# Optimization experiments

Hardware: AMD Instinct MI355X
Metric: run time of the kernel (lower is better)

## Reference

```python
import jax, jax.numpy as jnp
import numpy as np

N_NODES = 50000
N_EDGES = 800000


def setup_inputs() -> dict:
    key = jax.random.key(0)
    k1, k2, k3, k4 = jax.random.split(key, 4)
    x = jax.random.normal(k1, (N_NODES, 128), dtype=jnp.float32)
    edge_index = jax.random.randint(k2, (2, N_EDGES), 0, N_NODES, dtype=jnp.int64)
    W1 = jax.random.normal(k3, (128, 64), dtype=jnp.float32) / np.sqrt(128.0)
    b1 = jnp.zeros((64,), dtype=jnp.float32)
    W2 = jax.random.normal(k4, (64, 40), dtype=jnp.float32) / np.sqrt(64.0)
    b2 = jnp.zeros((40,), dtype=jnp.float32)
    return {"x": x, "edge_index": edge_index, "W1": W1, "b1": b1, "W2": W2, "b2": b2}


def _gcn_norm(edge_index, n_nodes):
    # Add self-loops, then compute symmetric normalization D^{-1/2} A D^{-1/2}
    loop = jnp.arange(n_nodes, dtype=edge_index.dtype)
    row = jnp.concatenate([edge_index[0], loop])  # source
    col = jnp.concatenate([edge_index[1], loop])  # target
    ones = jnp.ones(row.shape[0], dtype=jnp.float32)
    deg = jax.ops.segment_sum(ones, col, num_segments=n_nodes)
    dinv = jnp.where(deg > 0, jax.lax.rsqrt(deg), 0.0)
    norm = dinv[row] * dinv[col]  # [E + N]
    return row, col, norm


def _gcn_conv(h, W, b, row, col, norm, n_nodes):
    hw = h @ W                         # transform first (smaller messages)
    msg = hw[row] * norm[:, None]      # gather + scale per edge
    agg = jax.ops.segment_sum(msg, col, num_segments=n_nodes)
    return agg + b


def reference(x, edge_index, W1, b1, W2, b2):
    n = x.shape[0]
    row, col, norm = _gcn_norm(edge_index, n)
    h = _gcn_conv(x, W1, b1, row, col, norm, n)
    h = jax.nn.relu(h)
    h = _gcn_conv(h, W2, b2, row, col, norm, n)
    return jax.nn.softmax(h, axis=-1)
```

## Files before the change

kernel.cpp:

```cpp
#include <hip/hip_runtime.h>
#include <hip/hip_fp16.h>

#define N_NODES 50000
#define N_EDGES 800000
#define F_IN   128
#define F_MID  64
#define F_OUT  40

#define SLICE_SHIFT 8
#define SLICE_SZ    256
#define NSLICE      196
#define PCHUNKS     256
#define PCHUNK_E    ((N_EDGES + PCHUNKS - 1) / PCHUNKS)
#define NCOUNT      (NSLICE * PCHUNKS)


__global__ __launch_bounds__(256) void bucket_count(const int* __restrict__ ei,
                                                    int* __restrict__ counts) {
    __shared__ int cnt[NSLICE];
    if (threadIdx.x < NSLICE) cnt[threadIdx.x] = 0;
    __syncthreads();
    int e0 = blockIdx.x * PCHUNK_E;
    int e1 = e0 + PCHUNK_E; if (e1 > N_EDGES) e1 = N_EDGES;
    for (int e = e0 + threadIdx.x; e < e1; e += 256) {
        int c = ei[N_EDGES + e];
        atomicAdd(&cnt[c >> SLICE_SHIFT], 1);
    }
    __syncthreads();
    if (threadIdx.x < NSLICE) counts[threadIdx.x * PCHUNKS + blockIdx.x] = cnt[threadIdx.x];
}


__global__ __launch_bounds__(256) void sc_scan(const int* __restrict__ counts,
                                               int* __restrict__ choff) {
    __shared__ int T[256];
    __shared__ int P[256];
    __shared__ int ws[4];
    int tid = threadIdx.x, b = blockIdx.x;
    int lane = tid & 63, wv = tid >> 6;

    for (int r = wv; r < NSLICE; r += 4) {
        const int* row = counts + r * PCHUNKS;
        int ssum = row[lane] + row[lane + 64] + row[lane + 128] + row[lane + 192];
#pragma unroll
        for (int off = 32; off > 0; off >>= 1) ssum += __shfl_xor(ssum, off, 64);
        if (lane == 0) T[r] = ssum;
    }
    if (tid >= NSLICE && tid < 256) T[tid] = 0;
    __syncthreads();

    int v = T[tid];
    int inc = v;
#pragma unroll
    for (int st = 1; st < 64; st <<= 1) {
        int t = __shfl_up(inc, st, 64);
        if (lane >= st) inc += t;
    }
    if (lane == 63) ws[wv] = inc;
    __syncthreads();
    int woff = 0;
    for (int w = 0; w < wv; ++w) woff += ws[w];
    P[tid] = woff + inc - v;
    __syncthreads();
    int base_b = P[b];

    __syncthreads();
    int c = counts[b * PCHUNKS + tid];
    inc = c;
#pragma unroll
    for (int st = 1; st < 64; st <<= 1) {
        int t = __shfl_up(inc, st, 64);
        if (lane >= st) inc += t;
    }
    if (lane == 63) ws[wv] = inc;
    __syncthreads();
    woff = 0;
    for (int w = 0; w < wv; ++w) woff += ws[w];
    choff[b * PCHUNKS + tid] = base_b + woff + inc - c;
}


__global__ __launch_bounds__(256) void bucket_scatter(const int* __restrict__ ei,
                                                      const int* __restrict__ choff,
                                                      int* __restrict__ pairs) {
    __shared__ int cur[NSLICE];
    if (threadIdx.x < NSLICE) cur[threadIdx.x] = choff[threadIdx.x * PCHUNKS + blockIdx.x];
    __syncthreads();
    int e0 = blockIdx.x * PCHUNK_E;
    int e1 = e0 + PCHUNK_E; if (e1 > N_EDGES) e1 = N_EDGES;
    for (int e = e0 + threadIdx.x; e < e1; e += 256) {
        int r = ei[e];
        int c = ei[N_EDGES + e];
        int pos = atomicAdd(&cur[c >> SLICE_SHIFT], 1);
        pairs[pos] = r | ((c & (SLICE_SZ - 1)) << 16);
    }
}


__global__ __launch_bounds__(256) void slice_csr_gemm1(const int* __restrict__ pairs,
                                                       const int* __restrict__ choff,
                                                       const float* __restrict__ x,
                                                       const float* __restrict__ W1,
                                                       int* __restrict__ rowptr,
                                                       float* __restrict__ dinv,
                                                       int* __restrict__ srcs,
                                                       __half* __restrict__ hw1h) {
    __shared__ int hist[SLICE_SZ];
    __shared__ int wpart[4];
    __shared__ float sdinv[SLICE_SZ];
    __shared__ float sW[F_IN * F_MID];
    __shared__ float sX[64][68];
    int s = blockIdx.x;
    int base = choff[s * PCHUNKS];
    int end  = (s == NSLICE - 1) ? N_EDGES : choff[(s + 1) * PCHUNKS];
    int tid = threadIdx.x;
    hist[tid] = 0;
    __syncthreads();
    for (int i = base + tid; i < end; i += 256)
        atomicAdd(&hist[pairs[i] >> 16], 1);
    __syncthreads();
    int v = hist[tid];
    int lane = tid & 63, wv = tid >> 6;
    int inc = v;
#pragma unroll
    for (int st = 1; st < 64; st <<= 1) {
        int t = __shfl_up(inc, st, 64);
        if (lane >= st) inc += t;
    }
    if (lane == 63) wpart[wv] = inc;
    __syncthreads();
    int woff = 0;
    for (int w = 0; w < wv; ++w) woff += wpart[w];
    int ex = woff + inc - v;
    __syncthreads();
    hist[tid] = ex;
    float dv = rsqrtf((float)v + 1.0f);
    sdinv[tid] = dv;
    int node = s * SLICE_SZ + tid;
    if (node < N_NODES) {
        rowptr[node] = base + ex;
        dinv[node]   = dv;
    }
    if (node == N_NODES - 1) rowptr[N_NODES] = N_EDGES;
    __syncthreads();
    for (int i = base + tid; i < end; i += 256) {
        int p = pairs[i];
        int pos = atomicAdd(&hist[p >> 16], 1);
        srcs[base + pos] = p & 0xFFFF;
    }

    const float4* W4 = (const float4*)W1;
    float4* sW4 = (float4*)sW;
    for (int i = tid; i < F_IN * F_MID / 4; i += 256) sW4[i] = W4[i];

    int tx = tid & 15, ty = tid >> 4;
    int c0 = tx * 4, r0 = ty * 4;
    int sBase = s * SLICE_SZ;

    for (int sub = 0; sub < 4; ++sub) {
        int row0 = sBase + sub * 64;
        float acc[4][4] = {};
        for (int p = 0; p < 2; ++p) {
            __syncthreads();
#pragma unroll
            for (int it = 0; it < 4; ++it) {
                int i = (tid + it * 256) * 4;
                int r = i >> 6, k = i & 63;
                float4 vx = make_float4(0.f, 0.f, 0.f, 0.f);
                if (row0 + r < N_NODES)
                    vx = *(const float4*)&x[(size_t)(row0 + r) * F_IN + p * 64 + k];
                *(float4*)&sX[r][k] = vx;
            }
            __syncthreads();
            const float* sWp = sW + p * 64 * F_MID;
#pragma unroll 4
            for (int k = 0; k < 64; ++k) {
                float4 w = *(const float4*)&sWp[k * F_MID + c0];
                float a0 = sX[r0 + 0][k];
                float a1 = sX[r0 + 1][k];
                float a2 = sX[r0 + 2][k];
                float a3 = sX[r0 + 3][k];
                acc[0][0] = fmaf(a0, w.x, acc[0][0]); acc[0][1] = fmaf(a0, w.y, acc[0][1]);
                acc[0][2] = fmaf(a0, w.z, acc[0][2]); acc[0][3] = fmaf(a0, w.w, acc[0][3]);
                acc[1][0] = fmaf(a1, w.x, acc[1][0]); acc[1][1] = fmaf(a1, w.y, acc[1][1]);
                acc[1][2] = fmaf(a1, w.z, acc[1][2]); acc[1][3] = fmaf(a1, w.w, acc[1][3]);
                acc[2][0] = fmaf(a2, w.x, acc[2][0]); acc[2][1] = fmaf(a2, w.y, acc[2][1]);
                acc[2][2] = fmaf(a2, w.z, acc[2][2]); acc[2][3] = fmaf(a2, w.w, acc[2][3]);
                acc[3][0] = fmaf(a3, w.x, acc[3][0]); acc[3][1] = fmaf(a3, w.y, acc[3][1]);
                acc[3][2] = fmaf(a3, w.z, acc[3][2]); acc[3][3] = fmaf(a3, w.w, acc[3][3]);
            }
        }
#pragma unroll
        for (int j = 0; j < 4; ++j) {
            int row = row0 + r0 + j;
            if (row < N_NODES) {
                float d = sdinv[sub * 64 + r0 + j];
                __half2 p0 = __floats2half2_rn(acc[j][0] * d, acc[j][1] * d);
                __half2 p1 = __floats2half2_rn(acc[j][2] * d, acc[j][3] * d);
                uint2 u = make_uint2(*reinterpret_cast<unsigned int*>(&p0),
                                     *reinterpret_cast<unsigned int*>(&p1));
                *reinterpret_cast<uint2*>(&hw1h[(size_t)row * F_MID + c0]) = u;
            }
        }
    }
}


__global__ __launch_bounds__(256) void gather1_kernel(const int* __restrict__ rowptr,
                                                      const int* __restrict__ srcs,
                                                      const __half* __restrict__ hw1h,
                                                      const float* __restrict__ dinv,
                                                      const float* __restrict__ b1,
                                                      float* __restrict__ h) {
    int n = blockIdx.x * 4 + (threadIdx.x >> 6);
    int lane = threadIdx.x & 63;
    if (n >= N_NODES) return;
    int s = __builtin_amdgcn_readfirstlane(rowptr[n]);
    int e = __builtin_amdgcn_readfirstlane(rowptr[n + 1]);
    const __half* hb = hw1h + lane;
    float acc = 0.f;
    int j = s;
    for (; j + 8 <= e; j += 8) {
        int i0 = srcs[j + 0], i1 = srcs[j + 1], i2 = srcs[j + 2], i3 = srcs[j + 3];
        int i4 = srcs[j + 4], i5 = srcs[j + 5], i6 = srcs[j + 6], i7 = srcs[j + 7];
        float v0 = __half2float(hb[(size_t)i0 << 6]);
        float v1 = __half2float(hb[(size_t)i1 << 6]);
        float v2 = __half2float(hb[(size_t)i2 << 6]);
        float v3 = __half2float(hb[(size_t)i3 << 6]);
        float v4 = __half2float(hb[(size_t)i4 << 6]);
        float v5 = __half2float(hb[(size_t)i5 << 6]);
        float v6 = __half2float(hb[(size_t)i6 << 6]);
        float v7 = __half2float(hb[(size_t)i7 << 6]);
        acc += ((v0 + v1) + (v2 + v3)) + ((v4 + v5) + (v6 + v7));
    }
    for (; j + 2 <= e; j += 2) {
        int i0 = srcs[j], i1 = srcs[j + 1];
        acc += __half2float(hb[(size_t)i0 << 6]) + __half2float(hb[(size_t)i1 << 6]);
    }
    if (j < e) acc += __half2float(hb[(size_t)srcs[j] << 6]);
    float d = dinv[n];
    float v = fmaf(d, acc + __half2float(hb[(size_t)n << 6]), b1[lane]);
    h[(size_t)n * F_MID + lane] = fmaxf(v, 0.f);
}


__global__ __launch_bounds__(256) void gemm2_kernel(const float* __restrict__ h,
                                                    const float* __restrict__ W2,
                                                    const float* __restrict__ dinv,
                                                    __half* __restrict__ hw2h) {
    __shared__ float sW[F_MID * F_OUT];
    for (int i = threadIdx.x; i < F_MID * F_OUT; i += 256) sW[i] = W2[i];
    __syncthreads();
    int idx = blockIdx.x * 256 + threadIdx.x;
    int r = idx >> 6;
    int c = idx & 63;
    float acc = 0.f;
    if (c < F_OUT) {
        const float* hr = h + (size_t)r * F_MID;
#pragma unroll
        for (int k = 0; k < F_MID; ++k) acc = fmaf(hr[k], sW[k * F_OUT + c], acc);
        acc *= dinv[r];
    }
    hw2h[idx] = __float2half(acc);
}


__global__ __launch_bounds__(256) void gather2_softmax_kernel(const int* __restrict__ rowptr,
                                                              const int* __restrict__ srcs,
                                                              const __half* __restrict__ hw2h,
                                                              const float* __restrict__ dinv,
                                                              const float* __restrict__ b2,
                                                              float* __restrict__ out) {
    int n = blockIdx.x * 4 + (threadIdx.x >> 6);
    int lane = threadIdx.x & 63;
    if (n >= N_NODES) return;
    int s = __builtin_amdgcn_readfirstlane(rowptr[n]);
    int e = __builtin_amdgcn_readfirstlane(rowptr[n + 1]);
    const __half* gb = hw2h + lane;
    float acc = 0.f;
    int j = s;
    for (; j + 8 <= e; j += 8) {
        int i0 = srcs[j + 0], i1 = srcs[j + 1], i2 = srcs[j + 2], i3 = srcs[j + 3];
        int i4 = srcs[j + 4], i5 = srcs[j + 5], i6 = srcs[j + 6], i7 = srcs[j + 7];
        float v0 = __half2float(gb[(size_t)i0 << 6]);
        float v1 = __half2float(gb[(size_t)i1 << 6]);
        float v2 = __half2float(gb[(size_t)i2 << 6]);
        float v3 = __half2float(gb[(size_t)i3 << 6]);
        float v4 = __half2float(gb[(size_t)i4 << 6]);
        float v5 = __half2float(gb[(size_t)i5 << 6]);
        float v6 = __half2float(gb[(size_t)i6 << 6]);
        float v7 = __half2float(gb[(size_t)i7 << 6]);
        acc += ((v0 + v1) + (v2 + v3)) + ((v4 + v5) + (v6 + v7));
    }
    for (; j + 2 <= e; j += 2) {
        int i0 = srcs[j], i1 = srcs[j + 1];
        acc += __half2float(gb[(size_t)i0 << 6]) + __half2float(gb[(size_t)i1 << 6]);
    }
    if (j < e) acc += __half2float(gb[(size_t)srcs[j] << 6]);
    float d = dinv[n];
    float v = -3.402823466e38f;
    if (lane < F_OUT)
        v = fmaf(d, acc + __half2float(gb[(size_t)n << 6]), b2[lane]);
    float m = v;
#pragma unroll
    for (int off = 32; off > 0; off >>= 1) m = fmaxf(m, __shfl_xor(m, off, 64));
    float p = (lane < F_OUT) ? __expf(v - m) : 0.f;
    float su = p;
#pragma unroll
    for (int off = 32; off > 0; off >>= 1) su += __shfl_xor(su, off, 64);
    if (lane < F_OUT) out[(size_t)n * F_OUT + lane] = p / su;
}


extern "C" void kernel_launch(void* const* d_in, const int* in_sizes, int n_in,
                              void* d_out, int out_size, void* d_ws, size_t ws_size,
                              hipStream_t stream) {
    const float* x  = (const float*)d_in[0];
    const int*   ei = (const int*)d_in[1];
    const float* W1 = (const float*)d_in[2];
    const float* b1 = (const float*)d_in[3];
    const float* W2 = (const float*)d_in[4];
    const float* b2 = (const float*)d_in[5];
    float* out = (float*)d_out;

    char* ws = (char*)d_ws;
    size_t off = 0;
    auto alloc = [&](size_t bytes) -> void* {
        void* p = ws + off;
        off += (bytes + 255) & ~(size_t)255;
        return p;
    };
    int*    counts = (int*)   alloc(NCOUNT * sizeof(int));
    int*    choff  = (int*)   alloc(NCOUNT * sizeof(int));
    int*    pairs  = (int*)   alloc((size_t)N_EDGES * sizeof(int));
    int*    rowptr = (int*)   alloc((N_NODES + 1) * sizeof(int));
    float*  dinv   = (float*) alloc(N_NODES * sizeof(float));
    int*    srcs   = (int*)   alloc((size_t)N_EDGES * sizeof(int));
    __half* hw1h   = (__half*)alloc((size_t)N_NODES * F_MID * sizeof(__half));
    float*  h      = (float*) alloc((size_t)N_NODES * F_MID * sizeof(float));
    __half* hw2h   = (__half*)alloc((size_t)N_NODES * F_MID * sizeof(__half));

    bucket_count   <<<PCHUNKS, 256, 0, stream>>>(ei, counts);
    sc_scan        <<<NSLICE, 256, 0, stream>>>(counts, choff);
    bucket_scatter <<<PCHUNKS, 256, 0, stream>>>(ei, choff, pairs);
    slice_csr_gemm1<<<NSLICE, 256, 0, stream>>>(pairs, choff, x, W1, rowptr, dinv, srcs, hw1h);
    gather1_kernel <<<(N_NODES + 3) / 4, 256, 0, stream>>>(rowptr, srcs, hw1h, dinv, b1, h);
    gemm2_kernel   <<<(N_NODES * F_MID) / 256, 256, 0, stream>>>(h, W2, dinv, hw2h);
    gather2_softmax_kernel<<<(N_NODES + 3) / 4, 256, 0, stream>>>(rowptr, srcs, hw2h, dinv, b2, out);
}
```

Before: 241.6 us.

## Split CSR build from GEMM1 and stage bucket scatter through shared memory

The fused slice_csr_gemm1 kernel ran on only 196 blocks, so the 128x64 GEMM over 50k nodes used few CUs. It is split into a slice_csr kernel and a separate gemm1 kernel with 782 blocks of 64 rows, which reads dinv from global memory. bucket_scatter now does a local prefix sum per chunk, sorts edges by slice in shared memory, and then writes pairs to global in contiguous runs instead of scattering them. The cost is one extra kernel launch and a round trip of dinv through global memory.

```diff
diff --git a/kernel.cpp b/kernel.cpp
--- a/kernel.cpp
+++ b/kernel.cpp
@@ -63,8 +63,8 @@
     P[tid] = woff + inc - v;
     __syncthreads();
     int base_b = P[b];
-
-    __syncthreads();
+    __syncthreads();
+
     int c = counts[b * PCHUNKS + tid];
     inc = c;
 #pragma unroll
@@ -81,35 +81,62 @@
 
 
 __global__ __launch_bounds__(256) void bucket_scatter(const int* __restrict__ ei,
+                                                      const int* __restrict__ counts,
                                                       const int* __restrict__ choff,
                                                       int* __restrict__ pairs) {
+    __shared__ int lofs[NSLICE];
     __shared__ int cur[NSLICE];
-    if (threadIdx.x < NSLICE) cur[threadIdx.x] = choff[threadIdx.x * PCHUNKS + blockIdx.x];
-    __syncthreads();
-    int e0 = blockIdx.x * PCHUNK_E;
+    __shared__ int delta[NSLICE];
+    __shared__ int wsp[4];
+    __shared__ int staged[PCHUNK_E];
+    __shared__ unsigned char sl[PCHUNK_E];
+    int tid = threadIdx.x, b = blockIdx.x;
+    int lane = tid & 63, wv = tid >> 6;
+
+    int c = (tid < NSLICE) ? counts[tid * PCHUNKS + b] : 0;
+    int inc = c;
+#pragma unroll
+    for (int st = 1; st < 64; st <<= 1) {
+        int t = __shfl_up(inc, st, 64);
+        if (lane >= st) inc += t;
+    }
+    if (lane == 63) wsp[wv] = inc;
+    __syncthreads();
+    int woff = 0;
+    for (int w = 0; w < wv; ++w) woff += wsp[w];
+    int ex = woff + inc - c;
+    if (tid < NSLICE) {
+        lofs[tid]  = ex;
+        cur[tid]   = ex;
+        delta[tid] = choff[tid * PCHUNKS + b] - ex;
+    }
+    __syncthreads();
+
+    int e0 = b * PCHUNK_E;
     int e1 = e0 + PCHUNK_E; if (e1 > N_EDGES) e1 = N_EDGES;
-    for (int e = e0 + threadIdx.x; e < e1; e += 256) {
+    int nE = e1 - e0;
+    for (int e = e0 + tid; e < e1; e += 256) {
         int r = ei[e];
-        int c = ei[N_EDGES + e];
-        int pos = atomicAdd(&cur[c >> SLICE_SHIFT], 1);
-        pairs[pos] = r | ((c & (SLICE_SZ - 1)) << 16);
-    }
-}
-
-
-__global__ __launch_bounds__(256) void slice_csr_gemm1(const int* __restrict__ pairs,
-                                                       const int* __restrict__ choff,
-                                                       const float* __restrict__ x,
-                                                       const float* __restrict__ W1,
-                                                       int* __restrict__ rowptr,
-                                                       float* __restrict__ dinv,
-                                                       int* __restrict__ srcs,
-                                                       __half* __restrict__ hw1h) {
+        int cc = ei[N_EDGES + e];
+        int s = cc >> SLICE_SHIFT;
+        int pos = atomicAdd(&cur[s], 1);
+        staged[pos] = r | ((cc & (SLICE_SZ - 1)) << 16);
+        sl[pos] = (unsigned char)s;
+    }
+    __syncthreads();
+
+    for (int t = tid; t < nE; t += 256)
+        pairs[delta[sl[t]] + t] = staged[t];
+}
+
+
+__global__ __launch_bounds__(256) void slice_csr(const int* __restrict__ pairs,
+                                                 const int* __restrict__ choff,
+                                                 int* __restrict__ rowptr,
+                                                 float* __restrict__ dinv,
+                                                 int* __restrict__ srcs) {
     __shared__ int hist[SLICE_SZ];
     __shared__ int wpart[4];
-    __shared__ float sdinv[SLICE_SZ];
-    __shared__ float sW[F_IN * F_MID];
-    __shared__ float sX[64][68];
     int s = blockIdx.x;
     int base = choff[s * PCHUNKS];
     int end  = (s == NSLICE - 1) ? N_EDGES : choff[(s + 1) * PCHUNKS];
@@ -134,12 +161,10 @@
     int ex = woff + inc - v;
     __syncthreads();
     hist[tid] = ex;
-    float dv = rsqrtf((float)v + 1.0f);
-    sdinv[tid] = dv;
     int node = s * SLICE_SZ + tid;
     if (node < N_NODES) {
         rowptr[node] = base + ex;
-        dinv[node]   = dv;
+        dinv[node]   = rsqrtf((float)v + 1.0f);
     }
     if (node == N_NODES - 1) rowptr[N_NODES] = N_EDGES;
     __syncthreads();
@@ -148,59 +173,65 @@
         int pos = atomicAdd(&hist[p >> 16], 1);
         srcs[base + pos] = p & 0xFFFF;
     }
-
+}
+
+
+__global__ __launch_bounds__(256) void gemm1_kernel(const float* __restrict__ x,
+                                                    const float* __restrict__ W1,
+                                                    const float* __restrict__ dinv,
+                                                    __half* __restrict__ hw1h) {
+    __shared__ float sW[F_IN * F_MID];
+    __shared__ float sX[64][68];
+    int tid = threadIdx.x;
     const float4* W4 = (const float4*)W1;
     float4* sW4 = (float4*)sW;
     for (int i = tid; i < F_IN * F_MID / 4; i += 256) sW4[i] = W4[i];
 
+    int row0 = blockIdx.x * 64;
     int tx = tid & 15, ty = tid >> 4;
     int c0 = tx * 4, r0 = ty * 4;
-    int sBase = s * SLICE_SZ;
-
-    for (int sub = 0; sub < 4; ++sub) {
-        int row0 = sBase + sub * 64;
-        float acc[4][4] = {};
-        for (int p = 0; p < 2; ++p) {
-            __syncthreads();
-#pragma unroll
-            for (int it = 0; it < 4; ++it) {
-                int i = (tid + it * 256) * 4;
-                int r = i >> 6, k = i & 63;
-                float4 vx = make_float4(0.f, 0.f, 0.f, 0.f);
-                if (row0 + r < N_NODES)
-                    vx = *(const float4*)&x[(size_t)(row0 + r) * F_IN + p * 64 + k];
-                *(float4*)&sX[r][k] = vx;
-            }
-            __syncthreads();
-            const float* sWp = sW + p * 64 * F_MID;
+    float acc[4][4] = {};
+
+    for (int p = 0; p < 2; ++p) {
+        __syncthreads();
+#pragma unroll
+        for (int it = 0; it < 4; ++it) {
+            int i = (tid + it * 256) * 4;
+            int r = i >> 6, k = i & 63;
+            float4 v = make_float4(0.f, 0.f, 0.f, 0.f);
+            if (row0 + r < N_NODES)
+                v = *(const float4*)&x[(size_t)(row0 + r) * F_IN + p * 64 + k];
+            *(float4*)&sX[r][k] = v;
+        }
+        __syncthreads();
+        const float* sWp = sW + p * 64 * F_MID;
 #pragma unroll 4
-            for (int k = 0; k < 64; ++k) {
-                float4 w = *(const float4*)&sWp[k * F_MID + c0];
-                float a0 = sX[r0 + 0][k];
-                float a1 = sX[r0 + 1][k];
-                float a2 = sX[r0 + 2][k];
-                float a3 = sX[r0 + 3][k];
-                acc[0][0] = fmaf(a0, w.x, acc[0][0]); acc[0][1] = fmaf(a0, w.y, acc[0][1]);
-                acc[0][2] = fmaf(a0, w.z, acc[0][2]); acc[0][3] = fmaf(a0, w.w, acc[0][3]);
-                acc[1][0] = fmaf(a1, w.x, acc[1][0]); acc[1][1] = fmaf(a1, w.y, acc[1][1]);
-                acc[1][2] = fmaf(a1, w.z, acc[1][2]); acc[1][3] = fmaf(a1, w.w, acc[1][3]);
-                acc[2][0] = fmaf(a2, w.x, acc[2][0]); acc[2][1] = fmaf(a2, w.y, acc[2][1]);
-                acc[2][2] = fmaf(a2, w.z, acc[2][2]); acc[2][3] = fmaf(a2, w.w, acc[2][3]);
-                acc[3][0] = fmaf(a3, w.x, acc[3][0]); acc[3][1] = fmaf(a3, w.y, acc[3][1]);
-                acc[3][2] = fmaf(a3, w.z, acc[3][2]); acc[3][3] = fmaf(a3, w.w, acc[3][3]);
-            }
+        for (int k = 0; k < 64; ++k) {
+            float4 w = *(const float4*)&sWp[k * F_MID + c0];
+            float a0 = sX[r0 + 0][k];
+            float a1 = sX[r0 + 1][k];
+            float a2 = sX[r0 + 2][k];
+            float a3 = sX[r0 + 3][k];
+            acc[0][0] = fmaf(a0, w.x, acc[0][0]); acc[0][1] = fmaf(a0, w.y, acc[0][1]);
+            acc[0][2] = fmaf(a0, w.z, acc[0][2]); acc[0][3] = fmaf(a0, w.w, acc[0][3]);
+            acc[1][0] = fmaf(a1, w.x, acc[1][0]); acc[1][1] = fmaf(a1, w.y, acc[1][1]);
+            acc[1][2] = fmaf(a1, w.z, acc[1][2]); acc[1][3] = fmaf(a1, w.w, acc[1][3]);
+            acc[2][0] = fmaf(a2, w.x, acc[2][0]); acc[2][1] = fmaf(a2, w.y, acc[2][1]);
+            acc[2][2] = fmaf(a2, w.z, acc[2][2]); acc[2][3] = fmaf(a2, w.w, acc[2][3]);
+            acc[3][0] = fmaf(a3, w.x, acc[3][0]); acc[3][1] = fmaf(a3, w.y, acc[3][1]);
+            acc[3][2] = fmaf(a3, w.z, acc[3][2]); acc[3][3] = fmaf(a3, w.w, acc[3][3]);
         }
-#pragma unroll
-        for (int j = 0; j < 4; ++j) {
-            int row = row0 + r0 + j;
-            if (row < N_NODES) {
-                float d = sdinv[sub * 64 + r0 + j];
-                __half2 p0 = __floats2half2_rn(acc[j][0] * d, acc[j][1] * d);
-                __half2 p1 = __floats2half2_rn(acc[j][2] * d, acc[j][3] * d);
-                uint2 u = make_uint2(*reinterpret_cast<unsigned int*>(&p0),
-                                     *reinterpret_cast<unsigned int*>(&p1));
-                *reinterpret_cast<uint2*>(&hw1h[(size_t)row * F_MID + c0]) = u;
-            }
+    }
+#pragma unroll
+    for (int j = 0; j < 4; ++j) {
+        int row = row0 + r0 + j;
+        if (row < N_NODES) {
+            float d = dinv[row];
+            __half2 p0 = __floats2half2_rn(acc[j][0] * d, acc[j][1] * d);
+            __half2 p1 = __floats2half2_rn(acc[j][2] * d, acc[j][3] * d);
+            uint2 u = make_uint2(*reinterpret_cast<unsigned int*>(&p0),
+                                 *reinterpret_cast<unsigned int*>(&p1));
+            *reinterpret_cast<uint2*>(&hw1h[(size_t)row * F_MID + c0]) = u;
         }
     }
 }
@@ -340,11 +371,12 @@
     float*  h      = (float*) alloc((size_t)N_NODES * F_MID * sizeof(float));
     __half* hw2h   = (__half*)alloc((size_t)N_NODES * F_MID * sizeof(__half));
 
-    bucket_count   <<<PCHUNKS, 256, 0, stream>>>(ei, counts);
-    sc_scan        <<<NSLICE, 256, 0, stream>>>(counts, choff);
-    bucket_scatter <<<PCHUNKS, 256, 0, stream>>>(ei, choff, pairs);
-    slice_csr_gemm1<<<NSLICE, 256, 0, stream>>>(pairs, choff, x, W1, rowptr, dinv, srcs, hw1h);
-    gather1_kernel <<<(N_NODES + 3) / 4, 256, 0, stream>>>(rowptr, srcs, hw1h, dinv, b1, h);
-    gemm2_kernel   <<<(N_NODES * F_MID) / 256, 256, 0, stream>>>(h, W2, dinv, hw2h);
+    bucket_count  <<<PCHUNKS, 256, 0, stream>>>(ei, counts);
+    sc_scan       <<<NSLICE, 256, 0, stream>>>(counts, choff);
+    bucket_scatter<<<PCHUNKS, 256, 0, stream>>>(ei, counts, choff, pairs);
+    slice_csr     <<<NSLICE, 256, 0, stream>>>(pairs, choff, rowptr, dinv, srcs);
+    gemm1_kernel  <<<(N_NODES + 63) / 64, 256, 0, stream>>>(x, W1, dinv, hw1h);
+    gather1_kernel<<<(N_NODES + 3) / 4, 256, 0, stream>>>(rowptr, srcs, hw1h, dinv, b1, h);
+    gemm2_kernel  <<<(N_NODES * F_MID) / 256, 256, 0, stream>>>(h, W2, dinv, hw2h);
     gather2_softmax_kernel<<<(N_NODES + 3) / 4, 256, 0, stream>>>(rowptr, srcs, hw2h, dinv, b2, out);
 }
```

Result: faster. 231.1 us (-4.4%).
